# Kernel optimization log

Hardware: AMD Instinct MI355X
Metric: run time of the kernel (lower is better)

Reference implementation:

```python
import jax, jax.numpy as jnp
import numpy as np

B, T, C = 2, 2048, 1024
NH = 16
HD = C // NH

def build_alibi_bias(n_head, max_len):
    slopes = jnp.arange(1, n_head + 1, dtype=jnp.float32) / n_head  # [nh]
    ar = jnp.arange(max_len, dtype=jnp.float32)
    # bias[h, i, j] = slopes[h] * (j - i)
    return slopes[:, None, None] * (ar[None, None, :] - ar[None, :, None])

def setup_inputs() -> dict:
    key = jax.random.key(0)
    ks = jax.random.split(key, 7)
    s = 0.02
    return {
        "x": jax.random.normal(ks[0], (B, T, C), dtype=jnp.float32),
        "q_w": jax.random.normal(ks[1], (C, C), dtype=jnp.float32) * s,   # [in, out]
        "q_b": jnp.zeros((C,), dtype=jnp.float32),
        "kv_w": jax.random.normal(ks[2], (C, 2 * C), dtype=jnp.float32) * s,
        "kv_b": jnp.zeros((2 * C,), dtype=jnp.float32),
        "o_w": jax.random.normal(ks[3], (C, C), dtype=jnp.float32) * s,
        "o_b": jnp.zeros((C,), dtype=jnp.float32),
    }

def reference(x, q_w, q_b, kv_w, kv_b, o_w, o_b):
    Bx, Tx, Cx = x.shape
    q = (x @ q_w + q_b).reshape(Bx, Tx, NH, HD).transpose(0, 2, 1, 3)      # [B,nh,T,hd]
    kv = (x @ kv_w + kv_b).reshape(Bx, Tx, 2, NH, HD).transpose(2, 0, 3, 1, 4)
    k, v = kv[0], kv[1]                                                     # [B,nh,T,hd]
    att = jnp.einsum("bhqd,bhkd->bhqk", q, k) * (1.0 / np.sqrt(HD))        # [B,nh,T,T]
    att = att + build_alibi_bias(NH, Tx)[None]                              # ALiBi bias
    causal = jnp.tril(jnp.ones((Tx, Tx), dtype=bool))
    att = jnp.where(causal[None, None], att, -jnp.inf)
    att = jax.nn.softmax(att, axis=-1)
    y = jnp.einsum("bhqk,bhkd->bhqd", att, v)                               # [B,nh,T,hd]
    y = y.transpose(0, 2, 1, 3).reshape(Bx, Tx, Cx)
    return y @ o_w + o_b
```

## Files before the change

kernel.cpp:

```cpp
#include <hip/hip_runtime.h>
#include <hip/hip_bf16.h>

#define NB 2
#define NT 2048
#define NC 1024
#define NHD 16
#define HDD 64
#define LOG2E 1.4426950408889634f

typedef __attribute__((ext_vector_type(8))) short short8;
typedef __attribute__((ext_vector_type(4))) float f32x4;
typedef __attribute__((ext_vector_type(16))) float f32x16;

__device__ __forceinline__ ushort f2bf(float f) {
    union { float f; unsigned u; } v; v.f = f;
    unsigned u = v.u;
    unsigned r = (u + 0x7FFFu + ((u >> 16) & 1u)) >> 16;
    return (ushort)r;
}

__device__ __forceinline__ float bf2f(ushort u) {
    unsigned x = ((unsigned)u) << 16;
    float f; __builtin_memcpy(&f, &x, 4); return f;
}

__device__ __forceinline__ unsigned pkbf(float a, float b) {
    __hip_bfloat162 t = __float22bfloat162_rn(float2{a, b});
    unsigned u; __builtin_memcpy(&u, &t, 4); return u;
}

__device__ __forceinline__ void gload16(const ushort* g, ushort* l) {
    __builtin_amdgcn_global_load_lds((const __attribute__((address_space(1))) void*)g,
                                     (__attribute__((address_space(3))) void*)l, 16, 0, 0);
}

__device__ __forceinline__ void tcvt_tile(const float* __restrict__ src, ushort* __restrict__ dst,
                                          int Kd, int Nd, int kb, int nb)
{
    __shared__ ushort tile[64][68];
    const int tid = threadIdx.x;
    const int r = tid >> 2, c = (tid & 3) * 16;
    const float* sp = src + (size_t)(kb + r) * Nd + nb + c;
#pragma unroll
    for (int i = 0; i < 16; i += 4) {
        float4 v = *(const float4*)(sp + i);
        tile[r][c + i + 0] = f2bf(v.x);
        tile[r][c + i + 1] = f2bf(v.y);
        tile[r][c + i + 2] = f2bf(v.z);
        tile[r][c + i + 3] = f2bf(v.w);
    }
    __syncthreads();
    ushort* dp = dst + (size_t)(nb + r) * Kd + kb + c;
#pragma unroll
    for (int i = 0; i < 16; i += 8) {
        short8 o;
#pragma unroll
        for (int j = 0; j < 8; j++) o[j] = (short)tile[c + i + j][r];
        *(short8*)(dp + i) = o;
    }
}

__global__ __launch_bounds__(256)
void prep(const float* __restrict__ x, const float* __restrict__ q_w,
          const float* __restrict__ kv_w, const float* __restrict__ o_w,
          ushort* __restrict__ xb, ushort* __restrict__ wqkvT, ushort* __restrict__ woT)
{
    const int bid = blockIdx.x;
    if (bid < 2048) {
        int i = (bid * 256 + threadIdx.x) * 8;
        float4 a = *(const float4*)(x + i);
        float4 b = *(const float4*)(x + i + 4);
        short8 o;
        o[0] = (short)f2bf(a.x); o[1] = (short)f2bf(a.y);
        o[2] = (short)f2bf(a.z); o[3] = (short)f2bf(a.w);
        o[4] = (short)f2bf(b.x); o[5] = (short)f2bf(b.y);
        o[6] = (short)f2bf(b.z); o[7] = (short)f2bf(b.w);
        *(short8*)(xb + i) = o;
    } else if (bid < 2304) {
        int r = bid - 2048;
        tcvt_tile(q_w, wqkvT, 1024, 1024, (r & 15) * 64, (r >> 4) * 64);
    } else if (bid < 2816) {
        int r = bid - 2304;
        tcvt_tile(kv_w, wqkvT + 1024 * 1024, 1024, 2048, (r & 15) * 64, (r >> 4) * 64);
    } else {
        int r = bid - 2816;
        tcvt_tile(o_w, woT, 1024, 1024, (r & 15) * 64, (r >> 4) * 64);
    }
}

__global__ __launch_bounds__(256)
void vtr(const ushort* __restrict__ src, ushort* __restrict__ dst)
{
    __shared__ ushort tile[64][66];
    const int tid = threadIdx.x;
    const int bh = blockIdx.y;
    const int t0 = blockIdx.x * 64;
    const int r = tid >> 2, c = (tid & 3) * 16;
    const ushort* sp = src + ((size_t)bh * NT + t0 + r) * HDD + c;
    *(short8*)&tile[r][c]     = *(const short8*)sp;
    *(short8*)&tile[r][c + 8] = *(const short8*)(sp + 8);
    __syncthreads();
    ushort* dp = dst + ((size_t)bh * HDD + r) * NT + t0 + c;
    short8 o0, o1;
#pragma unroll
    for (int j = 0; j < 8; j++) { o0[j] = (short)tile[c + j][r]; o1[j] = (short)tile[c + 8 + j][r]; }
    *(short8*)dp = o0;
    *(short8*)(dp + 8) = o1;
}

template<int MODE>
__global__ __launch_bounds__(256)
void gemm128(const ushort* __restrict__ A, const ushort* __restrict__ Bt,
             const float* __restrict__ bias0, const float* __restrict__ bias1,
             ushort* __restrict__ Qo, ushort* __restrict__ Ko, ushort* __restrict__ Vo,
             float* __restrict__ Fo, int Kdim)
{
    __shared__ ushort Al[128 * 32];
    __shared__ ushort Bl[128 * 32];
    const int tid = threadIdx.x;
    const int lane = tid & 63, w = tid >> 6;
    const int wr = (w >> 1) * 64, wc = (w & 1) * 64;
    const int lg = lane >> 4, lc = lane & 15;
    const int bm = blockIdx.x * 128, bn = blockIdx.y * 128;

    f32x4 acc[4][4] = {};

    const int srow = lane >> 2, scol = (lane & 3) * 8;

    for (int k0 = 0; k0 < Kdim; k0 += 32) {
        __syncthreads();
#pragma unroll
        for (int c = 0; c < 2; c++) {
            int seg = w * 2 + c;
            int row = seg * 16 + srow;
            gload16(A  + (size_t)(bm + row) * Kdim + k0 + scol, &Al[seg * 512]);
            gload16(Bt + (size_t)(bn + row) * Kdim + k0 + scol, &Bl[seg * 512]);
        }
        __syncthreads();
        short8 af[4], bfv[4];
#pragma unroll
        for (int mt = 0; mt < 4; mt++) af[mt] = *(const short8*)&Al[(wr + mt*16 + lc) * 32 + lg*8];
#pragma unroll
        for (int nt = 0; nt < 4; nt++) bfv[nt] = *(const short8*)&Bl[(wc + nt*16 + lc) * 32 + lg*8];
#pragma unroll
        for (int mt = 0; mt < 4; mt++)
#pragma unroll
            for (int nt = 0; nt < 4; nt++)
                acc[mt][nt] = __builtin_amdgcn_mfma_f32_16x16x32_bf16(af[mt], bfv[nt], acc[mt][nt], 0, 0, 0);
    }

#pragma unroll
    for (int mt = 0; mt < 4; mt++) {
#pragma unroll
        for (int nt = 0; nt < 4; nt++) {
#pragma unroll
            for (int rr = 0; rr < 4; rr++) {
                int m = bm + wr + mt*16 + lg*4 + rr;
                int n = bn + wc + nt*16 + lc;
                float v = acc[mt][nt][rr];
                if (MODE == 0) {
                    int b = m >> 11, t = m & 2047;
                    if (n < NC) {
                        float q = (v + bias0[n]) * (0.125f * LOG2E);
                        int hh = n >> 6, d = n & 63;
                        Qo[(((size_t)b*NHD + hh)*NT + t)*HDD + d] = f2bf(q);
                    } else {
                        int j = n - NC;
                        float val = v + bias1[j];
                        int s = j >> 10;
                        int jj = j & 1023;
                        int hh = jj >> 6, d = jj & 63;
                        ushort* dst = s ? Vo : Ko;
                        dst[(((size_t)b*NHD + hh)*NT + t)*HDD + d] = f2bf(val);
                    }
                } else {
                    Fo[(size_t)m * NC + n] = v + bias0[n];
                }
            }
        }
    }
}

__global__ __launch_bounds__(256, 3)
void attn_fwd(const ushort* __restrict__ Q, const ushort* __restrict__ K,
              const ushort* __restrict__ Vt, ushort* __restrict__ Y,
              ushort* __restrict__ pool0, ushort* __restrict__ pool1,
              float* __restrict__ mlb)
{
    __shared__ ushort sb[2 * 64 * 72];
    ushort* Kl = sb;
    ushort* Vl = sb + 64 * 72;

    const int tid = threadIdx.x;
    const int lane = tid & 63, w = tid >> 6;
    const int lo5 = lane & 31, hi = lane >> 5;
    const int slot = (int)(blockIdx.x >> 5);
    const int bh = blockIdx.x & 31;
    const int b = bh >> 4, h = bh & 15;

    int qt, t_begin, t_end, pi = 0;
    const bool split = (slot < 26);
    if (split) {
        qt = 15 - (slot >> 1);
        const int s = slot & 1;
        t_begin = s * (qt + 1);
        t_end = t_begin + (qt + 1);
        pi = (bh * 13 + (qt - 3)) * 2 + s;
    } else {
        qt = 28 - slot;
        t_begin = 0;
        t_end = 2 * qt + 2;
    }

    const ushort* Qp = Q + (size_t)bh * NT * HDD;
    const ushort* Kp = K + (size_t)bh * NT * HDD;
    const ushort* Vp = Vt + (size_t)bh * HDD * NT;

    const int q0 = qt * 128 + w * 32;
    const int qlane = q0 + lo5;

    const float slope2 = (float)(h + 1) * (LOG2E / (float)NHD);

    short8 qf[4];
    {
        const ushort* qr = Qp + (size_t)qlane * HDD + 8 * hi;
#pragma unroll
        for (int kk = 0; kk < 4; kk++) qf[kk] = *(const short8*)(qr + kk * 16);
    }

    float bb[16];
#pragma unroll
    for (int r = 0; r < 16; r++) {
        int roff = (r & 3) + 8 * (r >> 2) + 4 * hi;
        bb[r] = slope2 * ((float)roff - (float)qlane);
    }

    float m_s = -1e30f, l_s = 0.f;
    f32x16 accO[2] = {};

    const int sr = tid >> 2, sd = (tid & 3) * 16;

    short8 pk0, pk1, pv0, pv1;
    {
        const ushort* kp = Kp + (size_t)(t_begin * 64 + sr) * HDD + sd;
        pk0 = *(const short8*)kp;
        pk1 = *(const short8*)(kp + 8);
        const ushort* vp = Vp + (size_t)sr * NT + t_begin * 64 + sd;
        pv0 = *(const short8*)vp;
        pv1 = *(const short8*)(vp + 8);
    }

    for (int t = t_begin; t < t_end; t++) {
        const int kv0 = t * 64;
        __syncthreads();
        *(short8*)&Kl[sr * 72 + sd]     = pk0;
        *(short8*)&Kl[sr * 72 + sd + 8] = pk1;
        *(short8*)&Vl[sr * 72 + sd]     = pv0;
        *(short8*)&Vl[sr * 72 + sd + 8] = pv1;
        __syncthreads();

        if (t + 1 < t_end) {
            const int kv1 = kv0 + 64;
            const ushort* kp = Kp + (size_t)(kv1 + sr) * HDD + sd;
            pk0 = *(const short8*)kp;
            pk1 = *(const short8*)(kp + 8);
            const ushort* vp = Vp + (size_t)sr * NT + kv1 + sd;
            pv0 = *(const short8*)vp;
            pv1 = *(const short8*)(vp + 8);
        }

#pragma unroll
        for (int sub = 0; sub < 2; sub++) {
            const int kv0s = kv0 + sub * 32;
            if (kv0s > q0 + 31) continue;

            f32x16 S = {};
            __builtin_amdgcn_s_setprio(1);
#pragma unroll
            for (int kk = 0; kk < 4; kk++) {
                short8 kf = *(const short8*)&Kl[(sub * 32 + lo5) * 72 + kk * 16 + 8 * hi];
                S = __builtin_amdgcn_mfma_f32_32x32x16_bf16(kf, qf[kk], S, 0, 0, 0);
            }
            __builtin_amdgcn_s_setprio(0);

            const float sk = slope2 * (float)kv0s;
            float mloc = m_s - sk;

            if (kv0s + 31 > q0) {
#pragma unroll
                for (int r = 0; r < 16; r++) {
                    int kvr = kv0s + (r & 3) + 8 * (r >> 2) + 4 * hi;
                    S[r] = (kvr > qlane) ? -1e30f : (S[r] + bb[r]);
                }
            } else {
#pragma unroll
                for (int r = 0; r < 16; r++) S[r] = S[r] + bb[r];
            }

            float rmax = S[0];
#pragma unroll
            for (int r = 1; r < 16; r++) rmax = fmaxf(rmax, S[r]);
            rmax = fmaxf(rmax, __shfl_xor(rmax, 32));

            if (__any(rmax - mloc > 8.0f)) {
                float mn = fmaxf(mloc, rmax);
                float sc = __builtin_amdgcn_exp2f(mloc - mn);
                mloc = mn;
                l_s *= sc;
#pragma unroll
                for (int dt = 0; dt < 2; dt++)
#pragma unroll
                    for (int r = 0; r < 16; r++) accO[dt][r] *= sc;
            }
            m_s = mloc + sk;

            float p[16], sum = 0.f;
#pragma unroll
            for (int r = 0; r < 16; r++) {
                p[r] = __builtin_amdgcn_exp2f(S[r] - mloc);
                sum += p[r];
            }
            sum += __shfl_xor(sum, 32);
            l_s += sum;

            unsigned pw[8], px[8];
#pragma unroll
            for (int i = 0; i < 8; i++) pw[i] = pkbf(p[2 * i], p[2 * i + 1]);
#pragma unroll
            for (int i = 0; i < 8; i++) px[i] = __shfl_xor(pw[i], 32);
            union { unsigned u[4]; short8 s; } fa0, fa1;
            fa0.u[0] = hi ? px[2] : pw[0];
            fa0.u[1] = hi ? px[3] : pw[1];
            fa0.u[2] = hi ? pw[2] : px[0];
            fa0.u[3] = hi ? pw[3] : px[1];
            fa1.u[0] = hi ? px[6] : pw[4];
            fa1.u[1] = hi ? px[7] : pw[5];
            fa1.u[2] = hi ? pw[6] : px[4];
            fa1.u[3] = hi ? pw[7] : px[5];

            __builtin_amdgcn_s_setprio(1);
#pragma unroll
            for (int dt = 0; dt < 2; dt++) {
                short8 vf0 = *(const short8*)&Vl[(dt * 32 + lo5) * 72 + sub * 32 + 8 * hi];
                short8 vf1 = *(const short8*)&Vl[(dt * 32 + lo5) * 72 + sub * 32 + 16 + 8 * hi];
                accO[dt] = __builtin_amdgcn_mfma_f32_32x32x16_bf16(vf0, fa0.s, accO[dt], 0, 0, 0);
                accO[dt] = __builtin_amdgcn_mfma_f32_32x32x16_bf16(vf1, fa1.s, accO[dt], 0, 0, 0);
            }
            __builtin_amdgcn_s_setprio(0);
        }
    }

    const float invl = split ? 1.0f : __builtin_amdgcn_rcpf(l_s);
    __syncthreads();
    ushort* myO = sb + w * 32 * 72;
#pragma unroll
    for (int dt = 0; dt < 2; dt++)
#pragma unroll
        for (int r = 0; r < 16; r++) {
            int d = dt * 32 + (r & 3) + 8 * (r >> 2) + 4 * hi;
            myO[lo5 * 72 + d] = f2bf(accO[dt][r] * invl);
        }
    if (split && hi == 0) {
        int rowin = w * 32 + lo5;
        mlb[pi * 256 + rowin] = m_s;
        mlb[pi * 256 + 128 + rowin] = l_s;
    }
    __syncthreads();
    const int orow = lane >> 1, ocol = (lane & 1) * 32;
    if (split) {
        ushort* pp = (pi < 512 ? pool0 + (size_t)pi * 8192 : pool1 + (size_t)(pi - 512) * 8192)
                     + (w * 32 + orow) * 64 + ocol;
#pragma unroll
        for (int c = 0; c < 4; c++)
            *(short8*)(pp + c * 8) = *(const short8*)&myO[orow * 72 + ocol + c * 8];
    } else {
        ushort* yp = Y + ((size_t)b * NT + q0 + orow) * NC + h * HDD + ocol;
#pragma unroll
        for (int c = 0; c < 4; c++)
            *(short8*)(yp + c * 8) = *(const short8*)&myO[orow * 72 + ocol + c * 8];
    }
}

__global__ __launch_bounds__(256)
void combine(const ushort* __restrict__ pool0, const ushort* __restrict__ pool1,
             const float* __restrict__ mlb, ushort* __restrict__ Y)
{
    const int cb = blockIdx.x;
    const int bh = cb / 13, qs = cb % 13;
    const int qt = qs + 3;
    const int b = bh >> 4, h = bh & 15;
    const int pi0 = (bh * 13 + qs) * 2, pi1 = pi0 + 1;

    const int tid = threadIdx.x;
    const int r = tid >> 1, c0 = (tid & 1) * 32;

    const float m0 = mlb[pi0 * 256 + r], l0 = mlb[pi0 * 256 + 128 + r];
    const float m1 = mlb[pi1 * 256 + r], l1 = mlb[pi1 * 256 + 128 + r];
    const float M = fmaxf(m0, m1);
    const float a0 = __builtin_amdgcn_exp2f(m0 - M);
    const float a1 = __builtin_amdgcn_exp2f(m1 - M);
    const float inv = __builtin_amdgcn_rcpf(a0 * l0 + a1 * l1);

    const ushort* p0 = (pi0 < 512 ? pool0 + (size_t)pi0 * 8192 : pool1 + (size_t)(pi0 - 512) * 8192) + r * 64 + c0;
    const ushort* p1 = (pi1 < 512 ? pool0 + (size_t)pi1 * 8192 : pool1 + (size_t)(pi1 - 512) * 8192) + r * 64 + c0;
    ushort* yp = Y + ((size_t)b * NT + qt * 128 + r) * NC + h * HDD + c0;

#pragma unroll
    for (int c = 0; c < 4; c++) {
        short8 u0 = *(const short8*)(p0 + c * 8);
        short8 u1 = *(const short8*)(p1 + c * 8);
        short8 o;
#pragma unroll
        for (int j = 0; j < 8; j++) {
            float v = (a0 * bf2f((ushort)u0[j]) + a1 * bf2f((ushort)u1[j])) * inv;
            o[j] = (short)f2bf(v);
        }
        *(short8*)(yp + c * 8) = o;
    }
}

extern "C" void kernel_launch(void* const* d_in, const int* in_sizes, int n_in,
                              void* d_out, int out_size, void* d_ws, size_t ws_size,
                              hipStream_t stream)
{
    const float* x    = (const float*)d_in[0];
    const float* q_w  = (const float*)d_in[1];
    const float* q_b  = (const float*)d_in[2];
    const float* kv_w = (const float*)d_in[3];
    const float* kv_b = (const float*)d_in[4];
    const float* o_w  = (const float*)d_in[5];
    const float* o_b  = (const float*)d_in[6];
    float* out = (float*)d_out;

    char* ws = (char*)d_ws;
    ushort* xb    = (ushort*)(ws);
    ushort* wqkvT = (ushort*)(ws + 8388608);
    ushort* woT   = (ushort*)(ws + 14680064);
    ushort* Qs    = (ushort*)(ws + 16777216);
    ushort* Ks    = (ushort*)(ws + 25165824);
    ushort* Vs    = (ushort*)(ws + 33554432);
    ushort* Ys    = (ushort*)(ws + 41943040);
    ushort* VsT   = xb;
    ushort* pool0 = Vs;
    ushort* pool1 = wqkvT;
    float*  mlb   = (float*)(ws + 8388608 + 5242880);

    prep<<<3072, 256, 0, stream>>>(x, q_w, kv_w, o_w, xb, wqkvT, woT);
    gemm128<0><<<dim3(32,24), 256, 0, stream>>>(xb, wqkvT, q_b, kv_b, Qs, Ks, Vs, nullptr, 1024);
    vtr<<<dim3(32,32), 256, 0, stream>>>(Vs, VsT);
    attn_fwd<<<928, 256, 0, stream>>>(Qs, Ks, VsT, Ys, pool0, pool1, mlb);
    combine<<<416, 256, 0, stream>>>(pool0, pool1, mlb, Ys);
    gemm128<1><<<dim3(32,8), 256, 0, stream>>>(Ys, woT, o_b, nullptr, nullptr, nullptr, nullptr, out, 1024);
}
```

Measured before the change: 142.1 us.

## Double-buffer LDS in GEMM and attention, remap GEMM blocks across XCDs

```diff
diff --git a/kernel.cpp b/kernel.cpp
--- a/kernel.cpp
+++ b/kernel.cpp
@@ -115,38 +115,53 @@
              ushort* __restrict__ Qo, ushort* __restrict__ Ko, ushort* __restrict__ Vo,
              float* __restrict__ Fo, int Kdim)
 {
-    __shared__ ushort Al[128 * 32];
-    __shared__ ushort Bl[128 * 32];
+    __shared__ ushort Al[2][128 * 32];
+    __shared__ ushort Bl[2][128 * 32];
     const int tid = threadIdx.x;
     const int lane = tid & 63, w = tid >> 6;
     const int wr = (w >> 1) * 64, wc = (w & 1) * 64;
     const int lg = lane >> 4, lc = lane & 15;
-    const int bm = blockIdx.x * 128, bn = blockIdx.y * 128;
+
+    const int nwg = gridDim.x;
+    const int cpx = nwg >> 3;
+    const int sid = (blockIdx.x & 7) * cpx + (blockIdx.x >> 3);
+    const int bm = (sid & 31) * 128, bn = (sid >> 5) * 128;
 
     f32x4 acc[4][4] = {};
 
     const int srow = lane >> 2, scol = (lane & 3) * 8;
-
+    const int seg0 = w * 2;
+
+    const ushort* apb = A  + (size_t)(bm + seg0 * 16 + srow) * Kdim + scol;
+    const ushort* bpb = Bt + (size_t)(bn + seg0 * 16 + srow) * Kdim + scol;
+
+    gload16(apb,              &Al[0][seg0 * 512]);
+    gload16(apb + 16 * Kdim,  &Al[0][(seg0 + 1) * 512]);
+    gload16(bpb,              &Bl[0][seg0 * 512]);
+    gload16(bpb + 16 * Kdim,  &Bl[0][(seg0 + 1) * 512]);
+
+    int cur = 0;
     for (int k0 = 0; k0 < Kdim; k0 += 32) {
         __syncthreads();
-#pragma unroll
-        for (int c = 0; c < 2; c++) {
-            int seg = w * 2 + c;
-            int row = seg * 16 + srow;
-            gload16(A  + (size_t)(bm + row) * Kdim + k0 + scol, &Al[seg * 512]);
-            gload16(Bt + (size_t)(bn + row) * Kdim + k0 + scol, &Bl[seg * 512]);
-        }
-        __syncthreads();
+        if (k0 + 32 < Kdim) {
+            gload16(apb + (k0 + 32),             &Al[cur ^ 1][seg0 * 512]);
+            gload16(apb + (k0 + 32) + 16 * Kdim, &Al[cur ^ 1][(seg0 + 1) * 512]);
+            gload16(bpb + (k0 + 32),             &Bl[cur ^ 1][seg0 * 512]);
+            gload16(bpb + (k0 + 32) + 16 * Kdim, &Bl[cur ^ 1][(seg0 + 1) * 512]);
+        }
         short8 af[4], bfv[4];
 #pragma unroll
-        for (int mt = 0; mt < 4; mt++) af[mt] = *(const short8*)&Al[(wr + mt*16 + lc) * 32 + lg*8];
-#pragma unroll
-        for (int nt = 0; nt < 4; nt++) bfv[nt] = *(const short8*)&Bl[(wc + nt*16 + lc) * 32 + lg*8];
+        for (int mt = 0; mt < 4; mt++) af[mt] = *(const short8*)&Al[cur][(wr + mt*16 + lc) * 32 + lg*8];
+#pragma unroll
+        for (int nt = 0; nt < 4; nt++) bfv[nt] = *(const short8*)&Bl[cur][(wc + nt*16 + lc) * 32 + lg*8];
+        __builtin_amdgcn_s_setprio(1);
 #pragma unroll
         for (int mt = 0; mt < 4; mt++)
 #pragma unroll
             for (int nt = 0; nt < 4; nt++)
                 acc[mt][nt] = __builtin_amdgcn_mfma_f32_16x16x32_bf16(af[mt], bfv[nt], acc[mt][nt], 0, 0, 0);
+        __builtin_amdgcn_s_setprio(0);
+        cur ^= 1;
     }
 
 #pragma unroll
@@ -187,9 +202,7 @@
               ushort* __restrict__ pool0, ushort* __restrict__ pool1,
               float* __restrict__ mlb)
 {
-    __shared__ ushort sb[2 * 64 * 72];
-    ushort* Kl = sb;
-    ushort* Vl = sb + 64 * 72;
+    __shared__ ushort sb[2 * 2 * 64 * 72];
 
     const int tid = threadIdx.x;
     const int lane = tid & 63, w = tid >> 6;
@@ -252,7 +265,8 @@
 
     for (int t = t_begin; t < t_end; t++) {
         const int kv0 = t * 64;
-        __syncthreads();
+        ushort* Kl = sb + ((t - t_begin) & 1) * 2 * 64 * 72;
+        ushort* Vl = Kl + 64 * 72;
         *(short8*)&Kl[sr * 72 + sd]     = pk0;
         *(short8*)&Kl[sr * 72 + sd + 8] = pk1;
         *(short8*)&Vl[sr * 72 + sd]     = pv0;
@@ -446,9 +460,9 @@
     float*  mlb   = (float*)(ws + 8388608 + 5242880);
 
     prep<<<3072, 256, 0, stream>>>(x, q_w, kv_w, o_w, xb, wqkvT, woT);
-    gemm128<0><<<dim3(32,24), 256, 0, stream>>>(xb, wqkvT, q_b, kv_b, Qs, Ks, Vs, nullptr, 1024);
+    gemm128<0><<<768, 256, 0, stream>>>(xb, wqkvT, q_b, kv_b, Qs, Ks, Vs, nullptr, 1024);
     vtr<<<dim3(32,32), 256, 0, stream>>>(Vs, VsT);
     attn_fwd<<<928, 256, 0, stream>>>(Qs, Ks, VsT, Ys, pool0, pool1, mlb);
     combine<<<416, 256, 0, stream>>>(pool0, pool1, mlb, Ys);
-    gemm128<1><<<dim3(32,8), 256, 0, stream>>>(Ys, woT, o_b, nullptr, nullptr, nullptr, nullptr, out, 1024);
-}
+    gemm128<1><<<256, 256, 0, stream>>>(Ys, woT, o_b, nullptr, nullptr, nullptr, nullptr, out, 1024);
+}
```

Result: faster. 137.7 us (-3.1%).
